# Performance work log

Measured on AMD Instinct MI355X. Metric: run time of the kernel, lower is better.

Reference implementation:

```python
import jax, jax.numpy as jnp
import numpy as np

NUM_HEADS = 4

def setup_inputs() -> dict:
    key = jax.random.key(0)
    ks = jax.random.split(key, 5)
    B, N, C = 2, 4096, 256
    s = 0.02
    return {
        "x": jax.random.normal(ks[0], (B, N, C), dtype=jnp.float32),
        "qkv_w": jax.random.normal(ks[1], (3 * C, C), dtype=jnp.float32) * s,
        "qkv_b": jax.random.normal(ks[2], (3 * C,), dtype=jnp.float32) * s,
        "out_w": jax.random.normal(ks[3], (C, C), dtype=jnp.float32) * s,
        "out_b": jax.random.normal(ks[4], (C,), dtype=jnp.float32) * s,
    }

def reference(x, qkv_w, qkv_b, out_w, out_b):
    # x: [B, N, C]; manual multi-head self-attention (eval mode, dropout off)
    B, N, C = x.shape
    H = NUM_HEADS
    D = C // H
    qkv = x @ qkv_w.T + qkv_b                      # [B, N, 3C]
    qkv = qkv.reshape(B, N, 3, H, D)
    qkv = jnp.transpose(qkv, (2, 0, 3, 1, 4))      # [3, B, H, N, D]
    q, k, v = qkv[0], qkv[1], qkv[2]
    scale = D ** -0.5
    attn = jnp.einsum('bhnd,bhmd->bhnm', q, k) * scale  # [B, H, N, N]
    attn = jax.nn.softmax(attn, axis=-1)
    out = jnp.einsum('bhnm,bhmd->bhnd', attn, v)   # [B, H, N, D]
    out = jnp.transpose(out, (0, 2, 1, 3)).reshape(B, N, C)
    return out @ out_w.T + out_b
```

## Files before the change

### kernel.cpp

```cpp
#include <hip/hip_runtime.h>

typedef __bf16 bf16x8 __attribute__((ext_vector_type(8)));
typedef float f32x4 __attribute__((ext_vector_type(4)));

#define MFMA_BF16(a, b, c) __builtin_amdgcn_mfma_f32_16x16x32_bf16((a), (b), (c), 0, 0, 0)

#define C1 0.18033688f

static __device__ __forceinline__ unsigned short f2bf(float f) {
    unsigned int u = __float_as_uint(f);
    unsigned int r = (u + 0x7fffu + ((u >> 16) & 1u)) >> 16;
    return (unsigned short)r;
}
static __device__ __forceinline__ float bf2f(unsigned short us) {
    return __uint_as_float(((unsigned int)us) << 16);
}
static __device__ __forceinline__ float exp2_hw(float x) {
    float r;
    asm("v_exp_f32 %0, %1" : "=v"(r) : "v"(x));
    return r;
}
static __device__ __forceinline__ unsigned pack_rh(float a, float b) {
    return __byte_perm(__float_as_uint(a) + 0x8000u, __float_as_uint(b) + 0x8000u, 0x7632);
}
static __device__ __forceinline__ void gload16(const void* g, void* l) {
    __builtin_amdgcn_global_load_lds(
        (const __attribute__((address_space(1))) unsigned int*)g,
        (__attribute__((address_space(3))) unsigned int*)l, 16, 0, 0);
}

__global__ __launch_bounds__(256) void convert_x_kernel(
    const void* __restrict__ x, unsigned short* __restrict__ xb) {
    const int lane = threadIdx.x & 63;
    int cnt = 0;
    {
        const unsigned short* sx = (const unsigned short*)x;
#pragma unroll
        for (int i = 0; i < 4; i++) {
            const int e = (sx[i * 64 + lane] >> 7) & 0xFF;
            cnt += __popcll(__ballot(e >= 195));
        }
    }
    const bool f32 = (cnt >= 8);
    const int base = blockIdx.x * 2048 + (int)threadIdx.x * 8;
    if (f32) {
        const float4 u0 = *(const float4*)((const float*)x + base);
        const float4 u1 = *(const float4*)((const float*)x + base + 4);
        uint4 p;
        p.x = pack_rh(u0.x, u0.y);
        p.y = pack_rh(u0.z, u0.w);
        p.z = pack_rh(u1.x, u1.y);
        p.w = pack_rh(u1.z, u1.w);
        *(uint4*)(xb + base) = p;
    } else {
        *(uint4*)(xb + base) = *(const uint4*)((const unsigned short*)x + base);
    }
}

template <bool QKV>
__global__ __launch_bounds__(256) void gemm_kernel(
    const unsigned short* __restrict__ A, const void* __restrict__ Wv,
    const void* __restrict__ biasv, unsigned short* __restrict__ Cb,
    float* __restrict__ Cf, unsigned short* __restrict__ Vt, int Nout) {
    constexpr int K = 256;
    __shared__ __align__(16) char sm[16384];

    const int tid = threadIdx.x;
    const int lane = tid & 63;
    const int wv = tid >> 6;
    const int m16 = lane & 15;
    const int quad = lane >> 4;
    const int bm = blockIdx.x * 64;
    const int bn = blockIdx.y * 64;

    int cnt = 0;
    {
        const unsigned short* sw = (const unsigned short*)Wv;
#pragma unroll
        for (int i = 0; i < 4; i++) {
            const int e = (sw[i * 64 + lane] >> 7) & 0xFF;
            cnt += __popcll(__ballot(e >= 195));
        }
    }
    const bool f32 = (cnt >= 8);

    int bgo[2], blo[2], brow[2], bchk[2];
#pragma unroll
    for (int i = 0; i < 2; i++) {
        const int c = wv * 128 + i * 64 + lane;
        const int r = c >> 3, g = (c & 7) ^ (r & 7);
        bgo[i] = r * (K * 2) + g * 16;
        blo[i] = c * 16;
        brow[i] = r;
        bchk[i] = g;
    }
    int bro[4][2];
#pragma unroll
    for (int t = 0; t < 4; t++)
#pragma unroll
        for (int ks = 0; ks < 2; ks++) {
            const int row = t * 16 + m16;
            bro[t][ks] = row * 64 + ((4 * ks + quad) ^ (m16 & 7)) * 8;
        }

    const char* bg = (const char*)Wv + (size_t)bn * K * 2;
    const float* Wf = (const float*)Wv;
    const unsigned short* ap = A + (size_t)(bm + wv * 16 + m16) * K + quad * 8;

    auto stageB = [&](int kb, int buf) {
        if (f32) {
#pragma unroll
            for (int i = 0; i < 2; i++) {
                const float* src = Wf + (size_t)(bn + brow[i]) * K + kb * 64 + bchk[i] * 8;
                const float4 u0 = *(const float4*)src;
                const float4 u1 = *(const float4*)(src + 4);
                uint4 p;
                p.x = pack_rh(u0.x, u0.y);
                p.y = pack_rh(u0.z, u0.w);
                p.z = pack_rh(u1.x, u1.y);
                p.w = pack_rh(u1.z, u1.w);
                *(uint4*)(sm + buf * 8192 + blo[i]) = p;
            }
        } else {
#pragma unroll
            for (int i = 0; i < 2; i++)
                gload16(bg + kb * 128 + bgo[i], sm + buf * 8192 + blo[i]);
        }
    };

    stageB(0, 0);
    bf16x8 a0 = *(const bf16x8*)(ap);
    bf16x8 a1 = *(const bf16x8*)(ap + 32);

    f32x4 acc[4] = {};
#pragma unroll
    for (int kb = 0; kb < 4; kb++) {
        __syncthreads();
        const int cur = kb & 1;
        bf16x8 a0n, a1n;
        if (kb < 3) {
            stageB(kb + 1, cur ^ 1);
            a0n = *(const bf16x8*)(ap + (kb + 1) * 64);
            a1n = *(const bf16x8*)(ap + (kb + 1) * 64 + 32);
        }
        const unsigned short* Blds = (const unsigned short*)(sm + cur * 8192);
#pragma unroll
        for (int ks = 0; ks < 2; ks++) {
            const bf16x8 a = ks ? a1 : a0;
#pragma unroll
            for (int t = 0; t < 4; t++) {
                const bf16x8 b = *(const bf16x8*)(Blds + bro[t][ks]);
                acc[t] = MFMA_BF16(a, b, acc[t]);
            }
        }
        if (kb < 3) {
            a0 = a0n;
            a1 = a1n;
        }
    }

    const float* bf_ = (const float*)biasv;
    const unsigned short* bh_ = (const unsigned short*)biasv;

    if (QKV && bn >= 512) {
        __syncthreads();
        unsigned short* tr = (unsigned short*)sm;
        const int lr = wv * 16 + quad * 4;
#pragma unroll
        for (int t = 0; t < 4; t++) {
            const int col = bn + t * 16 + m16;
            const float bv = f32 ? bf_[col] : bf2f(bh_[col]);
            uint2 w;
            w.x = pack_rh(acc[t][0] + bv, acc[t][1] + bv);
            w.y = pack_rh(acc[t][2] + bv, acc[t][3] + bv);
            *(uint2*)&tr[(t * 16 + m16) * 72 + lr] = w;
        }
        __syncthreads();
        const int d = tid >> 2;
        const int ch = (tid & 3) * 16;
        const uint4 o4a = *(const uint4*)&tr[d * 72 + ch];
        const uint4 o4b = *(const uint4*)&tr[d * 72 + ch + 8];
        const int hh = (bn - 512) >> 6;
        const int bb = bm >> 12, n0 = bm & 4095;
        const int nn = n0 + ch;
        const int kt = nn >> 7, koff = nn & 127;
        unsigned short* vdst =
            &Vt[(size_t)(((bb * 4 + hh) * 32 + kt) * 64 + d) * 128 + koff];
        *(uint4*)(vdst) = o4a;
        *(uint4*)(vdst + 8) = o4b;
        return;
    }

    const int row0 = bm + wv * 16 + quad * 4;
#pragma unroll
    for (int t = 0; t < 4; t++) {
        const int col = bn + t * 16 + m16;
        const float bv = f32 ? bf_[col] : bf2f(bh_[col]);
        float v[4];
#pragma unroll
        for (int r = 0; r < 4; r++) v[r] = acc[t][r] + bv;
        if (QKV) {
            const float sc = (col < 256) ? C1 : 1.0f;
#pragma unroll
            for (int r = 0; r < 4; r++)
                Cb[(size_t)(row0 + r) * 768 + col] = f2bf(v[r] * sc);
        } else {
            if (f32) {
#pragma unroll
                for (int r = 0; r < 4; r++) Cf[(size_t)(row0 + r) * Nout + col] = v[r];
            } else {
#pragma unroll
                for (int r = 0; r < 4; r++) Cb[(size_t)(row0 + r) * Nout + col] = f2bf(v[r]);
            }
        }
    }
}

#define ZERO_S(S)                                                     \
    do {                                                              \
        _Pragma("unroll") for (int mb = 0; mb < 2; mb++)              \
            _Pragma("unroll") for (int j = 0; j < 4; j++)             \
                S[mb][j] = (f32x4){0.f, 0.f, 0.f, 0.f};               \
    } while (0)

#define QKT(S, KBASE)                                                          \
    do {                                                                       \
        const unsigned short* Kb_ = (const unsigned short*)(KBASE);            \
        __builtin_amdgcn_s_setprio(1);                                         \
        _Pragma("unroll") for (int mb = 0; mb < 2; mb++)                       \
            _Pragma("unroll") for (int ks = 0; ks < 2; ks++) {                 \
                const bf16x8 ka_ = *(const bf16x8*)(Kb_ + kro[mb][ks]);        \
                _Pragma("unroll") for (int j = 0; j < 4; j++)                  \
                    S[mb][j] = MFMA_BF16(ka_, qf[j][ks], S[mb][j]);            \
            }                                                                  \
        __builtin_amdgcn_s_setprio(0);                                         \
    } while (0)

#define EXPP(S, PA)                                                            \
    do {                                                                       \
        _Pragma("unroll") for (int j = 0; j < 4; j++) {                        \
            const float e0 = exp2_hw(S[0][j][0]);                              \
            const float e1 = exp2_hw(S[0][j][1]);                              \
            const float e2 = exp2_hw(S[0][j][2]);                              \
            const float e3 = exp2_hw(S[0][j][3]);                              \
            const float e4 = exp2_hw(S[1][j][0]);                              \
            const float e5 = exp2_hw(S[1][j][1]);                              \
            const float e6 = exp2_hw(S[1][j][2]);                              \
            const float e7 = exp2_hw(S[1][j][3]);                              \
            uint4 pw_;                                                         \
            pw_.x = pack_rh(e0, e1);                                           \
            pw_.y = pack_rh(e2, e3);                                           \
            pw_.z = pack_rh(e4, e5);                                           \
            pw_.w = pack_rh(e6, e7);                                           \
            PA[j] = *(const bf16x8*)&pw_;                                      \
        }                                                                      \
    } while (0)

#define PVACC(PA, VBASE)                                                       \
    do {                                                                       \
        const unsigned short* Vb_ = (const unsigned short*)(VBASE);            \
        __builtin_amdgcn_s_setprio(1);                                         \
        _Pragma("unroll") for (int j = 0; j < 4; j++)                          \
            o1[j] = MFMA_BF16(PA[j], ones, o1[j]);                             \
        _Pragma("unroll") for (int t = 0; t < 4; t++) {                        \
            const uint2 va_ = *(const uint2*)(Vb_ + vroA[t]);                  \
            const uint2 vc_ = *(const uint2*)(Vb_ + (vroA[t] ^ 16));           \
            uint4 vv_;                                                         \
            vv_.x = va_.x;                                                     \
            vv_.y = va_.y;                                                     \
            vv_.z = vc_.x;                                                     \
            vv_.w = vc_.y;                                                     \
            const bf16x8 vb_ = *(const bf16x8*)&vv_;                           \
            _Pragma("unroll") for (int j = 0; j < 4; j++)                      \
                o[j][t] = MFMA_BF16(PA[j], vb_, o[j][t]);                      \
        }                                                                      \
        __builtin_amdgcn_s_setprio(0);                                         \
    } while (0)

#define GLK(DST)                                                               \
    {                                                                          \
        _Pragma("unroll") for (int i = 0; i < 4; i++)                          \
            gload16(kgn + kgo[i], (DST) + klo[i]);                             \
        kgn += 196608;                                                         \
    }
#define GLV(DST)                                                               \
    {                                                                          \
        _Pragma("unroll") for (int i = 0; i < 4; i++)                          \
            gload16(vgn + vgo[i], (DST) + vlo[i]);                             \
        vgn += 16384;                                                          \
    }

__global__ __launch_bounds__(256, 2) void attn_kernel(
    const unsigned short* __restrict__ qkv, const unsigned short* __restrict__ Vt,
    unsigned short* __restrict__ attn, int iters) {
    const int N = 4096, C3 = 768;
    __shared__ __align__(16) char sm[65536];

    const int tid = threadIdx.x;
    const int lane = tid & 63;
    const int wv = tid >> 6;
    const int m16 = lane & 15;
    const int quad = lane >> 4;

    const int bh = blockIdx.x & 7;
    const int qt = blockIdx.x >> 3;
    const int b = bh >> 2, h = bh & 3;

    bf16x8 qf[4][2];
#pragma unroll
    for (int j = 0; j < 4; j++)
#pragma unroll
        for (int ks = 0; ks < 2; ks++)
            qf[j][ks] = *(const bf16x8*)(qkv + ((size_t)b * N + qt * 64 + j * 16 + m16) * C3 +
                                         h * 64 + ks * 32 + quad * 8);

    uint4 ones_u;
    ones_u.x = ones_u.y = ones_u.z = ones_u.w = 0x3F803F80u;
    const bf16x8 ones = *(const bf16x8*)&ones_u;

    int kgo[4], vgo[4], klo[4], vlo[4];
#pragma unroll
    for (int i = 0; i < 4; i++) {
        const int c = i * 64 + lane;
        const int r = c >> 3, g = (c & 7) ^ (r & 7);
        kgo[i] = (wv * 32 + r) * 1536 + g * 16;
        klo[i] = c * 16;
        const int d = c >> 2, js = c & 3, jg = js ^ ((d >> 2) & 3);
        vgo[i] = d * 256 + wv * 64 + jg * 16;
        vlo[i] = c * 16;
    }
    int kro[2][2];
#pragma unroll
    for (int mb = 0; mb < 2; mb++)
#pragma unroll
        for (int ks = 0; ks < 2; ks++) {
            const int row = mb * 16 + m16;
            kro[mb][ks] = row * 64 + ((4 * ks + quad) ^ (m16 & 7)) * 8;
        }
    int vroA[4];
#pragma unroll
    for (int t = 0; t < 4; t++) {
        const int d = t * 16 + m16;
        const int c0 = (quad >> 1) ^ ((d >> 2) & 3);
        vroA[t] = d * 32 + c0 * 8 + (quad & 1) * 4;
    }

    char* Kreg0 = sm + wv * 8192;
    char* Vreg0 = sm + 32768 + wv * 8192;

    const char* kgp = (const char*)(qkv + (size_t)b * N * C3 + 256 + h * 64);
    const char* vgp = (const char*)(Vt + (size_t)bh * 262144);

#pragma unroll
    for (int i = 0; i < 4; i++) gload16(kgp + kgo[i], Kreg0 + klo[i]);
#pragma unroll
    for (int i = 0; i < 4; i++) gload16(vgp + vgo[i], Vreg0 + vlo[i]);
#pragma unroll
    for (int i = 0; i < 4; i++) gload16(kgp + 196608 + kgo[i], Kreg0 + 4096 + klo[i]);
#pragma unroll
    for (int i = 0; i < 4; i++) gload16(vgp + 16384 + vgo[i], Vreg0 + 4096 + vlo[i]);
    const char* kgn = kgp + 2 * 196608;
    const char* vgn = vgp + 2 * 16384;

    f32x4 o[4][4] = {};
    f32x4 o1[4] = {};
    f32x4 sA[2][4], sB[2][4];
    bf16x8 pa[4];

    asm volatile("s_waitcnt vmcnt(12)" ::: "memory");
    ZERO_S(sA);
    QKT(sA, Kreg0);

    for (int t2 = 0; t2 < 15; ++t2) {
        asm volatile("s_waitcnt vmcnt(4)" ::: "memory");
        GLK(Kreg0);
        ZERO_S(sB);
        QKT(sB, Kreg0 + 4096);
        EXPP(sA, pa);
        PVACC(pa, Vreg0);
        asm volatile("s_waitcnt lgkmcnt(0)" ::: "memory");
        GLV(Vreg0);

        asm volatile("s_waitcnt vmcnt(4)" ::: "memory");
        GLK(Kreg0 + 4096);
        ZERO_S(sA);
        QKT(sA, Kreg0);
        EXPP(sB, pa);
        PVACC(pa, Vreg0 + 4096);
        asm volatile("s_waitcnt lgkmcnt(0)" ::: "memory");
        GLV(Vreg0 + 4096);
    }
    asm volatile("s_waitcnt vmcnt(4)" ::: "memory");
    ZERO_S(sB);
    QKT(sB, Kreg0 + 4096);
    EXPP(sA, pa);
    PVACC(pa, Vreg0);
    asm volatile("s_waitcnt vmcnt(0)" ::: "memory");
    EXPP(sB, pa);
    PVACC(pa, Vreg0 + 4096);

    __syncthreads();
    float* Ored = (float*)sm;
    float* lsum = (float*)(sm + 16384);
    if (m16 == 0) {
#pragma unroll
        for (int j = 0; j < 4; j++)
#pragma unroll
            for (int r = 0; r < 4; r++)
                lsum[wv * 64 + j * 16 + quad * 4 + r] = o1[j][r];
    }
    const int row = tid >> 4;
    const int col = (tid & 15) * 4;
#pragma unroll
    for (int j = 0; j < 4; j++) {
#pragma unroll
        for (int t = 0; t < 4; t++)
#pragma unroll
            for (int r = 0; r < 4; r++)
                Ored[(wv * 16 + quad * 4 + r) * 64 + t * 16 + m16] = o[j][t][r];
        __syncthreads();
        f32x4 sum = *(f32x4*)&Ored[row * 64 + col];
        sum += *(f32x4*)&Ored[1024 + row * 64 + col];
        sum += *(f32x4*)&Ored[2048 + row * 64 + col];
        sum += *(f32x4*)&Ored[3072 + row * 64 + col];
        const float lq = lsum[j * 16 + row] + lsum[64 + j * 16 + row] +
                         lsum[128 + j * 16 + row] + lsum[192 + j * 16 + row];
        const int n = qt * 64 + j * 16 + row;
        const float inv = 1.0f / lq;
        uint2 w;
        w.x = pack_rh(sum[0] * inv, sum[1] * inv);
        w.y = pack_rh(sum[2] * inv, sum[3] * inv);
        *(uint2*)&attn[((size_t)b * N + n) * 256 + h * 64 + col] = w;
        __syncthreads();
    }
}

extern "C" void kernel_launch(void* const* d_in, const int* in_sizes, int n_in,
                              void* d_out, int out_size, void* d_ws, size_t ws_size,
                              hipStream_t stream) {
    const int B = 2, N = 4096, H = 4;
    const int M = B * N;

    char* wsb = (char*)d_ws;
    unsigned short* qkv_ws  = (unsigned short*)wsb;
    unsigned short* Vt_ws   = qkv_ws + 6291456;
    unsigned short* attn_ws = Vt_ws + 2097152;
    unsigned short* xb      = attn_ws + 2097152;

    convert_x_kernel<<<1024, 256, 0, stream>>>(d_in[0], xb);

    gemm_kernel<true><<<dim3(M / 64, 768 / 64), 256, 0, stream>>>(
        xb, d_in[1], d_in[2], qkv_ws, nullptr, Vt_ws, 768);

    attn_kernel<<<512, 256, 0, stream>>>(qkv_ws, Vt_ws, attn_ws, 32);

    gemm_kernel<false><<<dim3(M / 64, 256 / 64), 256, 0, stream>>>(
        attn_ws, d_in[3], d_in[4], (unsigned short*)d_out, (float*)d_out, nullptr, 256);
}
```

Baseline: 132.6 us.

## Halve attention query tile to 32 rows and raise occupancy to four blocks per CU

The attention kernel now processes 32 query rows per block instead of 64, launches 1024 blocks, cuts shared memory to about 33KB and sets launch bounds to allow 4 blocks per CU. Each wave handles 16-key chunks in a simpler single-stage loop that loads K and V and waits on them within the same iteration, replacing the old two-stage software pipeline. The final reduction across waves is done in one pass with wider stores. The aim is more resident waves to hide latency and a better-filled grid. In exchange, K/V are re-read from global memory twice as often and there is less in-wave prefetch overlap.

```diff
diff --git a/kernel.cpp b/kernel.cpp
--- a/kernel.cpp
+++ b/kernel.cpp
@@ -216,85 +216,11 @@
     }
 }
 
-#define ZERO_S(S)                                                     \
-    do {                                                              \
-        _Pragma("unroll") for (int mb = 0; mb < 2; mb++)              \
-            _Pragma("unroll") for (int j = 0; j < 4; j++)             \
-                S[mb][j] = (f32x4){0.f, 0.f, 0.f, 0.f};               \
-    } while (0)
-
-#define QKT(S, KBASE)                                                          \
-    do {                                                                       \
-        const unsigned short* Kb_ = (const unsigned short*)(KBASE);            \
-        __builtin_amdgcn_s_setprio(1);                                         \
-        _Pragma("unroll") for (int mb = 0; mb < 2; mb++)                       \
-            _Pragma("unroll") for (int ks = 0; ks < 2; ks++) {                 \
-                const bf16x8 ka_ = *(const bf16x8*)(Kb_ + kro[mb][ks]);        \
-                _Pragma("unroll") for (int j = 0; j < 4; j++)                  \
-                    S[mb][j] = MFMA_BF16(ka_, qf[j][ks], S[mb][j]);            \
-            }                                                                  \
-        __builtin_amdgcn_s_setprio(0);                                         \
-    } while (0)
-
-#define EXPP(S, PA)                                                            \
-    do {                                                                       \
-        _Pragma("unroll") for (int j = 0; j < 4; j++) {                        \
-            const float e0 = exp2_hw(S[0][j][0]);                              \
-            const float e1 = exp2_hw(S[0][j][1]);                              \
-            const float e2 = exp2_hw(S[0][j][2]);                              \
-            const float e3 = exp2_hw(S[0][j][3]);                              \
-            const float e4 = exp2_hw(S[1][j][0]);                              \
-            const float e5 = exp2_hw(S[1][j][1]);                              \
-            const float e6 = exp2_hw(S[1][j][2]);                              \
-            const float e7 = exp2_hw(S[1][j][3]);                              \
-            uint4 pw_;                                                         \
-            pw_.x = pack_rh(e0, e1);                                           \
-            pw_.y = pack_rh(e2, e3);                                           \
-            pw_.z = pack_rh(e4, e5);                                           \
-            pw_.w = pack_rh(e6, e7);                                           \
-            PA[j] = *(const bf16x8*)&pw_;                                      \
-        }                                                                      \
-    } while (0)
-
-#define PVACC(PA, VBASE)                                                       \
-    do {                                                                       \
-        const unsigned short* Vb_ = (const unsigned short*)(VBASE);            \
-        __builtin_amdgcn_s_setprio(1);                                         \
-        _Pragma("unroll") for (int j = 0; j < 4; j++)                          \
-            o1[j] = MFMA_BF16(PA[j], ones, o1[j]);                             \
-        _Pragma("unroll") for (int t = 0; t < 4; t++) {                        \
-            const uint2 va_ = *(const uint2*)(Vb_ + vroA[t]);                  \
-            const uint2 vc_ = *(const uint2*)(Vb_ + (vroA[t] ^ 16));           \
-            uint4 vv_;                                                         \
-            vv_.x = va_.x;                                                     \
-            vv_.y = va_.y;                                                     \
-            vv_.z = vc_.x;                                                     \
-            vv_.w = vc_.y;                                                     \
-            const bf16x8 vb_ = *(const bf16x8*)&vv_;                           \
-            _Pragma("unroll") for (int j = 0; j < 4; j++)                      \
-                o[j][t] = MFMA_BF16(PA[j], vb_, o[j][t]);                      \
-        }                                                                      \
-        __builtin_amdgcn_s_setprio(0);                                         \
-    } while (0)
-
-#define GLK(DST)                                                               \
-    {                                                                          \
-        _Pragma("unroll") for (int i = 0; i < 4; i++)                          \
-            gload16(kgn + kgo[i], (DST) + klo[i]);                             \
-        kgn += 196608;                                                         \
-    }
-#define GLV(DST)                                                               \
-    {                                                                          \
-        _Pragma("unroll") for (int i = 0; i < 4; i++)                          \
-            gload16(vgn + vgo[i], (DST) + vlo[i]);                             \
-        vgn += 16384;                                                          \
-    }
-
-__global__ __launch_bounds__(256, 2) void attn_kernel(
+__global__ __launch_bounds__(256, 4) void attn_kernel(
     const unsigned short* __restrict__ qkv, const unsigned short* __restrict__ Vt,
     unsigned short* __restrict__ attn, int iters) {
     const int N = 4096, C3 = 768;
-    __shared__ __align__(16) char sm[65536];
+    __shared__ __align__(16) char sm[33280];
 
     const int tid = threadIdx.x;
     const int lane = tid & 63;
@@ -306,132 +232,175 @@
     const int qt = blockIdx.x >> 3;
     const int b = bh >> 2, h = bh & 3;
 
-    bf16x8 qf[4][2];
-#pragma unroll
-    for (int j = 0; j < 4; j++)
+    bf16x8 qf[2][2];
+#pragma unroll
+    for (int j = 0; j < 2; j++)
 #pragma unroll
         for (int ks = 0; ks < 2; ks++)
-            qf[j][ks] = *(const bf16x8*)(qkv + ((size_t)b * N + qt * 64 + j * 16 + m16) * C3 +
+            qf[j][ks] = *(const bf16x8*)(qkv + ((size_t)b * N + qt * 32 + j * 16 + m16) * C3 +
                                          h * 64 + ks * 32 + quad * 8);
 
     uint4 ones_u;
     ones_u.x = ones_u.y = ones_u.z = ones_u.w = 0x3F803F80u;
     const bf16x8 ones = *(const bf16x8*)&ones_u;
 
-    int kgo[4], vgo[4], klo[4], vlo[4];
-#pragma unroll
-    for (int i = 0; i < 4; i++) {
+    int kgo[2], klo[2], vgo[2], vlo[2];
+#pragma unroll
+    for (int i = 0; i < 2; i++) {
         const int c = i * 64 + lane;
         const int r = c >> 3, g = (c & 7) ^ (r & 7);
-        kgo[i] = (wv * 32 + r) * 1536 + g * 16;
+        kgo[i] = (wv * 16 + r) * 1536 + g * 16;
         klo[i] = c * 16;
-        const int d = c >> 2, js = c & 3, jg = js ^ ((d >> 2) & 3);
-        vgo[i] = d * 256 + wv * 64 + jg * 16;
+        const int d = c >> 1, js = c & 1, jg = js ^ ((d >> 2) & 1);
+        vgo[i] = d * 256 + wv * 32 + jg * 16;
         vlo[i] = c * 16;
     }
-    int kro[2][2];
-#pragma unroll
-    for (int mb = 0; mb < 2; mb++)
-#pragma unroll
-        for (int ks = 0; ks < 2; ks++) {
-            const int row = mb * 16 + m16;
-            kro[mb][ks] = row * 64 + ((4 * ks + quad) ^ (m16 & 7)) * 8;
-        }
-    int vroA[4];
+    int kro[2];
+#pragma unroll
+    for (int ks = 0; ks < 2; ks++)
+        kro[ks] = m16 * 64 + ((4 * ks + quad) ^ (m16 & 7)) * 8;
+    int vro[4];
 #pragma unroll
     for (int t = 0; t < 4; t++) {
         const int d = t * 16 + m16;
-        const int c0 = (quad >> 1) ^ ((d >> 2) & 3);
-        vroA[t] = d * 32 + c0 * 8 + (quad & 1) * 4;
-    }
-
-    char* Kreg0 = sm + wv * 8192;
-    char* Vreg0 = sm + 32768 + wv * 8192;
-
-    const char* kgp = (const char*)(qkv + (size_t)b * N * C3 + 256 + h * 64);
-    const char* vgp = (const char*)(Vt + (size_t)bh * 262144);
-
-#pragma unroll
-    for (int i = 0; i < 4; i++) gload16(kgp + kgo[i], Kreg0 + klo[i]);
-#pragma unroll
-    for (int i = 0; i < 4; i++) gload16(vgp + vgo[i], Vreg0 + vlo[i]);
-#pragma unroll
-    for (int i = 0; i < 4; i++) gload16(kgp + 196608 + kgo[i], Kreg0 + 4096 + klo[i]);
-#pragma unroll
-    for (int i = 0; i < 4; i++) gload16(vgp + 16384 + vgo[i], Vreg0 + 4096 + vlo[i]);
-    const char* kgn = kgp + 2 * 196608;
-    const char* vgn = vgp + 2 * 16384;
-
-    f32x4 o[4][4] = {};
-    f32x4 o1[4] = {};
-    f32x4 sA[2][4], sB[2][4];
-    bf16x8 pa[4];
-
-    asm volatile("s_waitcnt vmcnt(12)" ::: "memory");
-    ZERO_S(sA);
-    QKT(sA, Kreg0);
-
-    for (int t2 = 0; t2 < 15; ++t2) {
+        const int ch = (quad >> 1) ^ ((d >> 2) & 1);
+        vro[t] = d * 16 + ch * 8 + (quad & 1) * 4;
+    }
+
+    char* KA = sm + wv * 8192;
+    char* KB_ = KA + 2048;
+    char* VA = KA + 4096;
+    char* VB = KA + 6144;
+
+    const char* kgn = (const char*)(qkv + (size_t)b * N * C3 + 256 + h * 64);
+    const char* vgn = (const char*)(Vt + (size_t)bh * 262144);
+
+#pragma unroll
+    for (int i = 0; i < 2; i++) gload16(kgn + kgo[i], KA + klo[i]);
+#pragma unroll
+    for (int i = 0; i < 2; i++) gload16(kgn + 98304 + kgo[i], KB_ + klo[i]);
+#pragma unroll
+    for (int i = 0; i < 2; i++) gload16(vgn + vgo[i], VA + vlo[i]);
+#pragma unroll
+    for (int i = 0; i < 2; i++) gload16(vgn + 128 + vgo[i], VB + vlo[i]);
+    kgn += 2 * 98304;
+    vgn += 16384;
+
+    f32x4 o[2][4] = {};
+    f32x4 o1[2] = {};
+
+    for (int w = 0; w < 32; ++w) {
+        asm volatile("s_waitcnt vmcnt(6)" ::: "memory");
+        f32x4 sA[2] = {};
+        {
+            const unsigned short* Kb_ = (const unsigned short*)KA;
+            __builtin_amdgcn_s_setprio(1);
+#pragma unroll
+            for (int ks = 0; ks < 2; ks++) {
+                const bf16x8 ka = *(const bf16x8*)(Kb_ + kro[ks]);
+#pragma unroll
+                for (int j = 0; j < 2; j++) sA[j] = MFMA_BF16(ka, qf[j][ks], sA[j]);
+            }
+            __builtin_amdgcn_s_setprio(0);
+        }
         asm volatile("s_waitcnt vmcnt(4)" ::: "memory");
-        GLK(Kreg0);
-        ZERO_S(sB);
-        QKT(sB, Kreg0 + 4096);
-        EXPP(sA, pa);
-        PVACC(pa, Vreg0);
-        asm volatile("s_waitcnt lgkmcnt(0)" ::: "memory");
-        GLV(Vreg0);
-
-        asm volatile("s_waitcnt vmcnt(4)" ::: "memory");
-        GLK(Kreg0 + 4096);
-        ZERO_S(sA);
-        QKT(sA, Kreg0);
-        EXPP(sB, pa);
-        PVACC(pa, Vreg0 + 4096);
-        asm volatile("s_waitcnt lgkmcnt(0)" ::: "memory");
-        GLV(Vreg0 + 4096);
-    }
-    asm volatile("s_waitcnt vmcnt(4)" ::: "memory");
-    ZERO_S(sB);
-    QKT(sB, Kreg0 + 4096);
-    EXPP(sA, pa);
-    PVACC(pa, Vreg0);
-    asm volatile("s_waitcnt vmcnt(0)" ::: "memory");
-    EXPP(sB, pa);
-    PVACC(pa, Vreg0 + 4096);
+        f32x4 sB[2] = {};
+        {
+            const unsigned short* Kb_ = (const unsigned short*)KB_;
+            __builtin_amdgcn_s_setprio(1);
+#pragma unroll
+            for (int ks = 0; ks < 2; ks++) {
+                const bf16x8 ka = *(const bf16x8*)(Kb_ + kro[ks]);
+#pragma unroll
+                for (int j = 0; j < 2; j++) sB[j] = MFMA_BF16(ka, qf[j][ks], sB[j]);
+            }
+            __builtin_amdgcn_s_setprio(0);
+        }
+        bf16x8 pa[2];
+#pragma unroll
+        for (int j = 0; j < 2; j++) {
+            uint4 pw;
+            pw.x = pack_rh(exp2_hw(sA[j][0]), exp2_hw(sA[j][1]));
+            pw.y = pack_rh(exp2_hw(sA[j][2]), exp2_hw(sA[j][3]));
+            pw.z = pack_rh(exp2_hw(sB[j][0]), exp2_hw(sB[j][1]));
+            pw.w = pack_rh(exp2_hw(sB[j][2]), exp2_hw(sB[j][3]));
+            pa[j] = *(const bf16x8*)&pw;
+        }
+        asm volatile("s_waitcnt vmcnt(0)" ::: "memory");
+        {
+            const unsigned short* Va_ = (const unsigned short*)VA;
+            const unsigned short* Vb_ = (const unsigned short*)VB;
+            __builtin_amdgcn_s_setprio(1);
+#pragma unroll
+            for (int j = 0; j < 2; j++) o1[j] = MFMA_BF16(pa[j], ones, o1[j]);
+#pragma unroll
+            for (int td = 0; td < 4; td++) {
+                const uint2 va = *(const uint2*)(Va_ + vro[td]);
+                const uint2 vc = *(const uint2*)(Vb_ + vro[td]);
+                uint4 vv;
+                vv.x = va.x;
+                vv.y = va.y;
+                vv.z = vc.x;
+                vv.w = vc.y;
+                const bf16x8 vb = *(const bf16x8*)&vv;
+#pragma unroll
+                for (int j = 0; j < 2; j++) o[j][td] = MFMA_BF16(pa[j], vb, o[j][td]);
+            }
+            __builtin_amdgcn_s_setprio(0);
+        }
+        if (w + 1 < 32) {
+            asm volatile("s_waitcnt lgkmcnt(0)" ::: "memory");
+#pragma unroll
+            for (int i = 0; i < 2; i++) gload16(kgn + kgo[i], KA + klo[i]);
+#pragma unroll
+            for (int i = 0; i < 2; i++) gload16(kgn + 98304 + kgo[i], KB_ + klo[i]);
+#pragma unroll
+            for (int i = 0; i < 2; i++) gload16(vgn + vgo[i], VA + vlo[i]);
+#pragma unroll
+            for (int i = 0; i < 2; i++) gload16(vgn + 128 + vgo[i], VB + vlo[i]);
+            kgn += 2 * 98304;
+            vgn += 16384;
+        }
+    }
 
     __syncthreads();
     float* Ored = (float*)sm;
-    float* lsum = (float*)(sm + 16384);
+    float* lsum = (float*)(sm + 32768);
+#pragma unroll
+    for (int j = 0; j < 2; j++)
+#pragma unroll
+        for (int td = 0; td < 4; td++)
+#pragma unroll
+            for (int r = 0; r < 4; r++)
+                Ored[wv * 2048 + (j * 16 + quad * 4 + r) * 64 + td * 16 + m16] =
+                    o[j][td][r];
     if (m16 == 0) {
 #pragma unroll
-        for (int j = 0; j < 4; j++)
+        for (int j = 0; j < 2; j++)
 #pragma unroll
             for (int r = 0; r < 4; r++)
-                lsum[wv * 64 + j * 16 + quad * 4 + r] = o1[j][r];
-    }
-    const int row = tid >> 4;
-    const int col = (tid & 15) * 4;
-#pragma unroll
-    for (int j = 0; j < 4; j++) {
-#pragma unroll
-        for (int t = 0; t < 4; t++)
-#pragma unroll
-            for (int r = 0; r < 4; r++)
-                Ored[(wv * 16 + quad * 4 + r) * 64 + t * 16 + m16] = o[j][t][r];
-        __syncthreads();
-        f32x4 sum = *(f32x4*)&Ored[row * 64 + col];
-        sum += *(f32x4*)&Ored[1024 + row * 64 + col];
-        sum += *(f32x4*)&Ored[2048 + row * 64 + col];
-        sum += *(f32x4*)&Ored[3072 + row * 64 + col];
-        const float lq = lsum[j * 16 + row] + lsum[64 + j * 16 + row] +
-                         lsum[128 + j * 16 + row] + lsum[192 + j * 16 + row];
-        const int n = qt * 64 + j * 16 + row;
+                lsum[wv * 32 + j * 16 + quad * 4 + r] = o1[j][r];
+    }
+    __syncthreads();
+    {
+        const int q32 = tid >> 3;
+        const int dch = (tid & 7) * 8;
+        f32x4 s0 = {}, s1 = {};
+        float lq = 0.f;
+#pragma unroll
+        for (int w = 0; w < 4; w++) {
+            const float* src = &Ored[w * 2048 + q32 * 64 + dch];
+            s0 += *(const f32x4*)(src);
+            s1 += *(const f32x4*)(src + 4);
+            lq += lsum[w * 32 + q32];
+        }
         const float inv = 1.0f / lq;
-        uint2 w;
-        w.x = pack_rh(sum[0] * inv, sum[1] * inv);
-        w.y = pack_rh(sum[2] * inv, sum[3] * inv);
-        *(uint2*)&attn[((size_t)b * N + n) * 256 + h * 64 + col] = w;
-        __syncthreads();
+        uint4 wout;
+        wout.x = pack_rh(s0[0] * inv, s0[1] * inv);
+        wout.y = pack_rh(s0[2] * inv, s0[3] * inv);
+        wout.z = pack_rh(s1[0] * inv, s1[1] * inv);
+        wout.w = pack_rh(s1[2] * inv, s1[3] * inv);
+        *(uint4*)&attn[((size_t)b * N + qt * 32 + q32) * 256 + h * 64 + dch] = wout;
     }
 }
 
@@ -452,7 +421,7 @@
     gemm_kernel<true><<<dim3(M / 64, 768 / 64), 256, 0, stream>>>(
         xb, d_in[1], d_in[2], qkv_ws, nullptr, Vt_ws, 768);
 
-    attn_kernel<<<512, 256, 0, stream>>>(qkv_ws, Vt_ws, attn_ws, 32);
+    attn_kernel<<<1024, 256, 0, stream>>>(qkv_ws, Vt_ws, attn_ws, 32);
 
     gemm_kernel<false><<<dim3(M / 64, 256 / 64), 256, 0, stream>>>(
         attn_ws, d_in[3], d_in[4], (unsigned short*)d_out, (float*)d_out, nullptr, 256);
```

New measurement: 161.7 us. 21.9% more time.
